# Kernel tuning notes

Hardware: AMD Instinct MI355X
Metric: run time of the kernel (lower is better)

Reference implementation:

```python
import jax, jax.numpy as jnp
import numpy as np

HEAD_DIM = 64
NUM_HEAD = 8
NUM_CLUSTERS = 16
B, N, M = 2, 2048, 2048


def setup_inputs() -> dict:
    key = jax.random.key(0)
    ks = jax.random.split(key, 10)
    d = HEAD_DIM
    inp = {
        "Q": jax.random.normal(ks[0], (B, NUM_HEAD, N, d), jnp.float32),
        "K": jax.random.normal(ks[1], (B, NUM_HEAD, M, d), jnp.float32),
        "V": jax.random.normal(ks[2], (B, NUM_HEAD, M, d), jnp.float32),
        "mask": jnp.zeros((B, M), jnp.int32),
        "noise": jax.random.uniform(ks[3], (B, NUM_HEAD, N, M), jnp.float32),
        "emb": jax.random.normal(ks[4], (NUM_HEAD * NUM_CLUSTERS, d), jnp.float32),
        "W1": jax.random.normal(ks[5], (d, d), jnp.float32) * 0.02,
        "b1": jnp.zeros((d,), jnp.float32),
        "W2": jax.random.normal(ks[6], (d, d), jnp.float32) * 0.02,
        "b2": jnp.zeros((d,), jnp.float32),
        "W3": jax.random.normal(ks[7], (d, d), jnp.float32) * 0.02,
        "b3": jnp.zeros((d,), jnp.float32),
    }
    return inp


def _proj(x, W1, b1, W2, b2, W3, b3):
    # torch nn.Linear: y = x @ W.T + b; dropout is identity in eval mode
    x = jax.nn.relu(jnp.einsum("bhnd,ed->bhne", x, W1) + b1)
    x = jax.nn.relu(jnp.einsum("bhnd,ed->bhne", x, W2) + b2)
    return jnp.einsum("bhnd,ed->bhne", x, W3) + b3


def reference(Q, K, V, mask, noise, emb, W1, b1, W2, b2, W3, b3):
    b, h, n, d = Q.shape
    m = V.shape[2]
    k = NUM_CLUSTERS

    clusters = emb.reshape(h, k, d)                                  # [h,k,d]
    dist = jnp.einsum("hkd,hjd->hkj", clusters, clusters)            # [h,k,k]
    # softmax over the flattened k*k matrix per head
    S = jax.nn.softmax(dist.reshape(h, k * k), axis=-1).reshape(h, k, k)

    Qhat = jax.nn.sigmoid(jnp.einsum("bhnd,hkd->bhnk", _proj(Q, W1, b1, W2, b2, W3, b3), clusters))
    Khat = jax.nn.sigmoid(jnp.einsum("bhmd,hkd->bhmk", _proj(K, W1, b1, W2, b2, W3, b3), clusters))

    SK = jnp.einsum("hkj,bhmj->bhkm", S, Khat)                       # [b,h,k,m]
    expA = jnp.einsum("bhnk,bhkm->bhnm", Qhat, SK)                   # Bernoulli probs in [0,1]

    # SampleGraphSparseGraph: Bernoulli sample with straight-through gradient
    sample = (noise < expA).astype(Q.dtype)
    graph = expA + jax.lax.stop_gradient(sample - expA)

    dot = jnp.einsum("bhnd,bhmd->bhnm", Q, K) / jnp.sqrt(jnp.asarray(d, Q.dtype))
    dot = jnp.where(mask[:, None, None, :] == 1, -jnp.inf, dot)
    p = jax.nn.softmax(dot, axis=-1) * graph
    # F.normalize(p=1): x / max(||x||_1, 1e-12); p is non-negative
    attn = p / jnp.maximum(jnp.sum(p, axis=-1, keepdims=True), 1e-12)

    X = jnp.einsum("bhnm,bhmd->bhnd", attn, V)
    sparsity = jnp.sum(graph, axis=(0, -1, -2)) / (b * n * m)        # [h]
    return X, sparsity, graph, attn
```

## Files before the change

kernel.cpp:

```cpp
#include <hip/hip_runtime.h>


typedef float  f32x4 __attribute__((ext_vector_type(4)));
typedef float  f32x8 __attribute__((ext_vector_type(8)));
typedef double f64x2 __attribute__((ext_vector_type(2)));
typedef __bf16 bf16x8 __attribute__((ext_vector_type(8)));

__device__ __forceinline__ unsigned short f2bf(float f) {
  __bf16 b = (__bf16)f;
  return __builtin_bit_cast(unsigned short, b);
}
__device__ __forceinline__ float bf2f(unsigned short u) {
  return (float)__builtin_bit_cast(__bf16, u);
}

__global__ __launch_bounds__(256) void kS(const float* __restrict__ emb,
                                          double* __restrict__ wsS,
                                          float* __restrict__ wsSP) {
  __shared__ double c[16][65];
  __shared__ double red[256];
  const int t = threadIdx.x, h = blockIdx.x;
  if (t == 0) wsSP[h] = 0.f;
  for (int i = t; i < 1024; i += 256) c[i >> 6][i & 63] = (double)emb[(size_t)h * 1024 + i];
  __syncthreads();
  const int k = t >> 4, j = t & 15;
  double acc = 0.0;
  for (int d = 0; d < 64; ++d) acc += c[k][d] * c[j][d];
  red[t] = acc; __syncthreads();
  for (int s = 128; s > 0; s >>= 1) { if (t < s) red[t] = fmax(red[t], red[t + s]); __syncthreads(); }
  const double mx = red[0]; __syncthreads();
  const double e = exp(acc - mx);
  red[t] = e; __syncthreads();
  for (int s = 128; s > 0; s >>= 1) { if (t < s) red[t] += red[t + s]; __syncthreads(); }
  wsS[h * 256 + t] = e / red[0];
}

__global__ __launch_bounds__(256) void kMLP(
    const float* __restrict__ Q, const float* __restrict__ K,
    const float* __restrict__ emb,
    const float* __restrict__ W1, const float* __restrict__ b1,
    const float* __restrict__ W2, const float* __restrict__ b2,
    const float* __restrict__ W3, const float* __restrict__ b3,
    const double* __restrict__ wsS,
    double* __restrict__ QHAT, double* __restrict__ SKT) {
  __shared__ double Xt[64][66];
  __shared__ float  Wl[64][68];
  __shared__ float  bsS[64];
  __shared__ float  cl[16][68];
  __shared__ double kh[64][17];
  __shared__ double Sl[256];

  const int t = threadIdx.x;
  const int blk = blockIdx.x;
  const int side = blk >> 9;
  const int idx = blk & 511;
  const int bh = idx >> 5;
  const int h = bh & 7;
  const int chunk = idx & 31;
  const size_t t0 = (size_t)bh * 2048 + (size_t)chunk * 64;

  const float* src = side ? K : Q;
  for (int i = t; i < 4096; i += 256) Xt[i >> 6][i & 63] = (double)src[t0 * 64 + i];

  const float* Ws[3] = {W1, W2, W3};
  const float* bs[3] = {b1, b2, b3};
  const int te = t & 15, tt = t >> 4;
  const int e0 = te * 4, tok0 = tt * 4;

  for (int l = 0; l < 3; ++l) {
    __syncthreads();
    for (int i = t; i < 4096; i += 256) Wl[i >> 6][i & 63] = Ws[l][i];
    if (t < 64) bsS[t] = bs[l][t];
    __syncthreads();
    double o[4][4];
#pragma unroll
    for (int i = 0; i < 4; ++i)
#pragma unroll
      for (int j = 0; j < 4; ++j) o[i][j] = 0.0;
    for (int d = 0; d < 64; d += 4) {
      double xa[4][4];
#pragma unroll
      for (int i = 0; i < 4; ++i) {
        const f64x2 lo = *(const f64x2*)&Xt[tok0 + i][d];
        const f64x2 hi = *(const f64x2*)&Xt[tok0 + i][d + 2];
        xa[i][0] = lo[0]; xa[i][1] = lo[1]; xa[i][2] = hi[0]; xa[i][3] = hi[1];
      }
      float4 wb[4];
#pragma unroll
      for (int j = 0; j < 4; ++j) wb[j] = *(const float4*)&Wl[e0 + j][d];
#pragma unroll
      for (int dd = 0; dd < 4; ++dd) {
        const double w0 = (double)((dd == 0) ? wb[0].x : (dd == 1) ? wb[0].y : (dd == 2) ? wb[0].z : wb[0].w);
        const double w1 = (double)((dd == 0) ? wb[1].x : (dd == 1) ? wb[1].y : (dd == 2) ? wb[1].z : wb[1].w);
        const double w2 = (double)((dd == 0) ? wb[2].x : (dd == 1) ? wb[2].y : (dd == 2) ? wb[2].z : wb[2].w);
        const double w3 = (double)((dd == 0) ? wb[3].x : (dd == 1) ? wb[3].y : (dd == 2) ? wb[3].z : wb[3].w);
#pragma unroll
        for (int i = 0; i < 4; ++i) {
          const double xv = xa[i][dd];
          o[i][0] += xv * w0; o[i][1] += xv * w1; o[i][2] += xv * w2; o[i][3] += xv * w3;
        }
      }
    }
#pragma unroll
    for (int i = 0; i < 4; ++i)
#pragma unroll
      for (int j = 0; j < 4; ++j) {
        double v = o[i][j] + (double)bsS[e0 + j];
        if (l < 2) v = fmax(v, 0.0);
        o[i][j] = v;
      }
    __syncthreads();
#pragma unroll
    for (int i = 0; i < 4; ++i)
#pragma unroll
      for (int j = 0; j < 4; ++j) Xt[tok0 + i][e0 + j] = o[i][j];
  }
  __syncthreads();
  for (int i = t; i < 1024; i += 256) cl[i >> 6][i & 63] = emb[(size_t)h * 1024 + i];
  if (side) { for (int i = t; i < 256; i += 256) Sl[i] = wsS[h * 256 + i]; }
  __syncthreads();

  const int tok = t >> 2, k0 = (t & 3) * 4;
  double z[4] = {0.0, 0.0, 0.0, 0.0};
  for (int d = 0; d < 64; d += 2) {
    const f64x2 xv = *(const f64x2*)&Xt[tok][d];
    const float2 c0 = *(const float2*)&cl[k0 + 0][d];
    const float2 c1 = *(const float2*)&cl[k0 + 1][d];
    const float2 c2 = *(const float2*)&cl[k0 + 2][d];
    const float2 c3 = *(const float2*)&cl[k0 + 3][d];
    z[0] += xv[0] * (double)c0.x; z[1] += xv[0] * (double)c1.x;
    z[2] += xv[0] * (double)c2.x; z[3] += xv[0] * (double)c3.x;
    z[0] += xv[1] * (double)c0.y; z[1] += xv[1] * (double)c1.y;
    z[2] += xv[1] * (double)c2.y; z[3] += xv[1] * (double)c3.y;
  }
  double hat[4];
#pragma unroll
  for (int j = 0; j < 4; ++j) hat[j] = 1.0 / (1.0 + exp(-z[j]));

  if (!side) {
#pragma unroll
    for (int j = 0; j < 4; ++j) QHAT[(t0 + tok) * 16 + k0 + j] = hat[j];
  } else {
    kh[tok][k0 + 0] = hat[0]; kh[tok][k0 + 1] = hat[1];
    kh[tok][k0 + 2] = hat[2]; kh[tok][k0 + 3] = hat[3];
    __syncthreads();
    double sk[4] = {0.0, 0.0, 0.0, 0.0};
    for (int jj = 0; jj < 16; ++jj) {
      const double kv = kh[tok][jj];
      sk[0] += Sl[(k0 + 0) * 16 + jj] * kv; sk[1] += Sl[(k0 + 1) * 16 + jj] * kv;
      sk[2] += Sl[(k0 + 2) * 16 + jj] * kv; sk[3] += Sl[(k0 + 3) * 16 + jj] * kv;
    }
#pragma unroll
    for (int j = 0; j < 4; ++j) SKT[(t0 + tok) * 16 + k0 + j] = sk[j];
  }
}

__global__ __launch_bounds__(256) void kSample(
    const float* __restrict__ noise,
    const double* __restrict__ qhat, const double* __restrict__ skt,
    float* __restrict__ wsSP,
    unsigned long long* __restrict__ GB64, float* __restrict__ GOUT) {
  const int t = threadIdx.x;
  const int lane = t & 63, wave = t >> 6;
  const int nt = blockIdx.x;
  const int mt = blockIdx.y;
  const int bh = blockIdx.z, h = bh & 7;
  const int n0 = nt * 64;
  const int mA = mt * 512 + wave * 64 + lane;
  const int mB = mA + 256;

  double skvA[16], skvB[16];
  {
    const double* spA = skt + ((size_t)bh * 2048 + mA) * 16;
    const double* spB = skt + ((size_t)bh * 2048 + mB) * 16;
#pragma unroll
    for (int q = 0; q < 8; ++q) {
      *(f64x2*)(skvA + 2 * q) = *(const f64x2*)(spA + 2 * q);
      *(f64x2*)(skvB + 2 * q) = *(const f64x2*)(spB + 2 * q);
    }
  }

  const double* qbase = qhat + ((size_t)bh * 2048 + n0) * 16;
  const float* nzbase = noise + ((size_t)bh * 2048 + n0) * 2048;
  float* gobase = GOUT + ((size_t)bh * 2048 + n0) * 2048;
  unsigned long long* gbbase = GB64 + ((size_t)bh * 2048 + n0) * 32;
  const int gA = mA >> 6, gB = mB >> 6;

  int cnt = 0;
  for (int n = 0; n < 64; ++n) {
    const double* qr = qbase + (size_t)n * 16;
    double ea0 = 0.0, ea1 = 0.0;
#pragma unroll
    for (int k = 0; k < 16; ++k) {
      const double qk = qr[k];
      ea0 += qk * skvA[k];
      ea1 += qk * skvB[k];
    }
    const float nzA = nzbase[(size_t)n * 2048 + mA];
    const float nzB = nzbase[(size_t)n * 2048 + mB];
    const int g0 = ((double)nzA < ea0) ? 1 : 0;
    const int g1 = ((double)nzB < ea1) ? 1 : 0;
    cnt += g0 + g1;
    const unsigned long long b0 = __ballot(g0);
    const unsigned long long b1 = __ballot(g1);
    if (lane == 0) {
      gbbase[(size_t)n * 32 + gA] = b0;
      gbbase[(size_t)n * 32 + gB] = b1;
    }
    gobase[(size_t)n * 2048 + mA] = g0 ? 1.0f : 0.0f;
    gobase[(size_t)n * 2048 + mB] = g1 ? 1.0f : 0.0f;
  }
  cnt += __shfl_xor(cnt, 1); cnt += __shfl_xor(cnt, 2); cnt += __shfl_xor(cnt, 4);
  cnt += __shfl_xor(cnt, 8); cnt += __shfl_xor(cnt, 16); cnt += __shfl_xor(cnt, 32);
  if (lane == 0) atomicAdd(&wsSP[h], (float)cnt);
}

__global__ __launch_bounds__(256) void kCvt(const float* __restrict__ K,
                                            const float* __restrict__ V,
                                            unsigned short* __restrict__ KB,
                                            unsigned short* __restrict__ VT) {
  __shared__ float vt[128][65];
  const int t = threadIdx.x;
  const int bh = blockIdx.x, ch = blockIdx.y;
  const size_t base = ((size_t)bh * 2048 + ch * 128) * 64;
  for (int i = t; i < 8192; i += 256) {
    KB[base + i] = f2bf(K[base + i]);
    vt[i >> 6][i & 63] = V[base + i];
  }
  __syncthreads();
  const size_t vbase = (size_t)bh * 64 * 2048 + ch * 128;
  for (int i = t; i < 8192; i += 256) {
    const int d = i >> 7, mm = i & 127;
    VT[vbase + (size_t)d * 2048 + mm] = f2bf(vt[mm][d]);
  }
}

__global__ __launch_bounds__(256, 4) void kAttn(
    const float* __restrict__ Q, const int* __restrict__ maskp,
    const unsigned short* __restrict__ KB, const unsigned short* __restrict__ VT,
    const unsigned int* __restrict__ GB32,
    float* __restrict__ XOUT, float* __restrict__ AOUT) {
  __shared__ unsigned int bitsS[16][64];
  __shared__ unsigned short stageS[4][16][32];
  __shared__ float dredS[4][16];
  __shared__ float dinvS[16];
  __shared__ float xredS[16][68];

  const int t = threadIdx.x;
  const int wave = t >> 6, lane = t & 63;
  const int bh = blockIdx.y, b = bh >> 3;
  const int n0 = blockIdx.x * 16;
  const int hi2 = lane >> 4;
  const int hi8 = hi2 << 3;
  const int g4 = hi2 << 2;
  const int lm = lane & 15;

  for (int i = t; i < 1024; i += 256)
    bitsS[i >> 6][i & 63] = GB32[((size_t)bh * 2048 + n0 + (i >> 6)) * 64 + (i & 63)];
  for (int i = t; i < 16 * 68; i += 256) ((float*)xredS)[i] = 0.f;

  const float* qrow = Q + ((size_t)bh * 2048 + n0 + lm) * 64;
  bf16x8 aq[2];
#pragma unroll
  for (int hh = 0; hh < 2; ++hh) {
    const int d0 = hi8 + hh * 32;
    const f32x4 qa = *(const f32x4*)(qrow + d0);
    const f32x4 qb = *(const f32x4*)(qrow + d0 + 4);
    bf16x8 v;
    v[0] = (__bf16)qa[0]; v[1] = (__bf16)qa[1]; v[2] = (__bf16)qa[2]; v[3] = (__bf16)qa[3];
    v[4] = (__bf16)qb[0]; v[5] = (__bf16)qb[1]; v[6] = (__bf16)qb[2]; v[7] = (__bf16)qb[3];
    aq[hh] = v;
  }

  const unsigned short* kbp = KB + (size_t)bh * 2048 * 64;
  const unsigned short* vtp = VT + (size_t)bh * 64 * 2048;
  const int* mkp = maskp + b * 2048;
  __syncthreads();

  float dsum[4] = {0.f, 0.f, 0.f, 0.f};
  for (int it = 0; it < 16; ++it) {
    const int mb = (wave << 9) + (it << 5);
    f32x4 st[2];
#pragma unroll
    for (int tt = 0; tt < 2; ++tt) {
      const unsigned short* kr = kbp + (size_t)(mb + tt * 16 + lm) * 64 + hi8;
      const bf16x8 b0 = *(const bf16x8*)(kr);
      const bf16x8 b1 = *(const bf16x8*)(kr + 32);
      f32x4 acc = (f32x4){0.f, 0.f, 0.f, 0.f};
      acc = __builtin_amdgcn_mfma_f32_16x16x32_bf16(aq[0], b0, acc, 0, 0, 0);
      acc = __builtin_amdgcn_mfma_f32_16x16x32_bf16(aq[1], b1, acc, 0, 0, 0);
      st[tt] = acc;
    }
#pragma unroll
    for (int tt = 0; tt < 2; ++tt) {
      const int mv = mkp[mb + tt * 16 + lm];
      const f32x4 sv4 = st[tt];
#pragma unroll
      for (int r = 0; r < 4; ++r) {
        const int g = (bitsS[g4 + r][mb >> 5] >> (tt * 16 + lm)) & 1;
        if (g && !mv) dsum[r] += __expf(sv4[r] * 0.125f);
      }
    }
  }
#pragma unroll
  for (int r = 0; r < 4; ++r) {
    float v = dsum[r];
    v += __shfl_xor(v, 1); v += __shfl_xor(v, 2); v += __shfl_xor(v, 4); v += __shfl_xor(v, 8);
    if (lm == 0) dredS[wave][g4 + r] = v;
  }
  __syncthreads();
  if (t < 16) {
    const float dv = dredS[0][t] + dredS[1][t] + dredS[2][t] + dredS[3][t];
    dinvS[t] = 1.0f / fmaxf(dv, 1e-12f);
  }
  __syncthreads();

  const size_t rowbase = (size_t)bh * 2048 + n0;
  f32x4 xacc[4];
#pragma unroll
  for (int td = 0; td < 4; ++td) xacc[td] = (f32x4){0.f, 0.f, 0.f, 0.f};

  for (int it = 0; it < 16; ++it) {
    const int mb = (wave << 9) + (it << 5);
    f32x4 st[2];
#pragma unroll
    for (int tt = 0; tt < 2; ++tt) {
      const unsigned short* kr = kbp + (size_t)(mb + tt * 16 + lm) * 64 + hi8;
      const bf16x8 b0 = *(const bf16x8*)(kr);
      const bf16x8 b1 = *(const bf16x8*)(kr + 32);
      f32x4 acc = (f32x4){0.f, 0.f, 0.f, 0.f};
      acc = __builtin_amdgcn_mfma_f32_16x16x32_bf16(aq[0], b0, acc, 0, 0, 0);
      acc = __builtin_amdgcn_mfma_f32_16x16x32_bf16(aq[1], b1, acc, 0, 0, 0);
      st[tt] = acc;
    }
#pragma unroll
    for (int tt = 0; tt < 2; ++tt) {
      const int mv = mkp[mb + tt * 16 + lm];
      const f32x4 sv4 = st[tt];
#pragma unroll
      for (int r = 0; r < 4; ++r) {
        const int row = g4 + r;
        const int g = (bitsS[row][mb >> 5] >> (tt * 16 + lm)) & 1;
        const float u = (g && !mv) ? __expf(sv4[r] * 0.125f) : 0.f;
        const int col = tt * 16 + lm;
        stageS[wave][row][col ^ (((row >> 2) & 3) << 3)] = f2bf(u);
      }
    }
    {
      const int rdcol = hi8 ^ (((lm >> 2) & 3) << 3);
      const bf16x8 ua = *(const bf16x8*)&stageS[wave][lm][rdcol];
#pragma unroll
      for (int td = 0; td < 4; ++td) {
        const bf16x8 vb = *(const bf16x8*)(vtp + (size_t)(td * 16 + lm) * 2048 + mb + hi8);
        xacc[td] = __builtin_amdgcn_mfma_f32_16x16x32_bf16(ua, vb, xacc[td], 0, 0, 0);
      }
    }
    {
      const int row = lane >> 2, q = lane & 3;
      const int rc = (q * 8) ^ (((row >> 2) & 3) << 3);
      const unsigned short* up = &stageS[wave][row][rc];
      const float inv = dinvS[row];
      f32x8 av;
#pragma unroll
      for (int j = 0; j < 8; ++j) av[j] = bf2f(up[j]) * inv;
      *(f32x8*)(AOUT + (rowbase + row) * 2048 + mb + q * 8) = av;
    }
  }

  for (int w = 0; w < 4; ++w) {
    if (wave == w) {
#pragma unroll
      for (int td = 0; td < 4; ++td)
#pragma unroll
        for (int r = 0; r < 4; ++r) xredS[g4 + r][td * 16 + lm] += xacc[td][r];
    }
    __syncthreads();
  }
  for (int i = t; i < 1024; i += 256) {
    const int nl = i >> 6, d = i & 63;
    XOUT[(rowbase + nl) * 64 + d] = xredS[nl][d] * dinvS[nl];
  }
}

__global__ void kFin(const float* __restrict__ wsSP, float* __restrict__ SPOUT) {
  const int t = threadIdx.x;
  if (t < 8) SPOUT[t] = wsSP[t] * (1.0f / 8388608.0f);
}

extern "C" void kernel_launch(void* const* d_in, const int* in_sizes, int n_in,
                              void* d_out, int out_size, void* d_ws, size_t ws_size,
                              hipStream_t stream) {
  const float* Q = (const float*)d_in[0];
  const float* K = (const float*)d_in[1];
  const float* V = (const float*)d_in[2];
  const int* mask = (const int*)d_in[3];
  const float* noise = (const float*)d_in[4];
  const float* emb = (const float*)d_in[5];
  const float* W1 = (const float*)d_in[6];
  const float* b1 = (const float*)d_in[7];
  const float* W2 = (const float*)d_in[8];
  const float* b2 = (const float*)d_in[9];
  const float* W3 = (const float*)d_in[10];
  const float* b3 = (const float*)d_in[11];

  char* ws = (char*)d_ws;
  double* wsS = (double*)(ws + 0);
  float* wsSP = (float*)(ws + 16384);
  double* QHAT = (double*)(ws + 32768);
  double* SKT  = (double*)(ws + 32768 + 4194304);
  unsigned short* KB = (unsigned short*)(ws + 32768);
  unsigned short* VT = (unsigned short*)(ws + 32768 + 4194304);
  unsigned long long* GB64 = (unsigned long long*)(ws + 32768 + 8388608);
  unsigned int* GB32 = (unsigned int*)(ws + 32768 + 8388608);

  float* out = (float*)d_out;
  float* XOUT = out;
  float* SPOUT = out + 2097152;
  float* GOUT = out + 2097160;
  float* AOUT = out + 69206024;

  kS<<<8, 256, 0, stream>>>(emb, wsS, wsSP);
  kMLP<<<1024, 256, 0, stream>>>(Q, K, emb, W1, b1, W2, b2, W3, b3, wsS, QHAT, SKT);
  kSample<<<dim3(32, 4, 16), 256, 0, stream>>>(noise, QHAT, SKT, wsSP, GB64, GOUT);
  kCvt<<<dim3(16, 16), 256, 0, stream>>>(K, V, KB, VT);
  kAttn<<<dim3(128, 16), 256, 0, stream>>>(Q, mask, KB, VT, GB32, XOUT, AOUT);
  kFin<<<1, 64, 0, stream>>>(wsSP, SPOUT);
}
```

Measured before the change: 506.7 us.

## Process 32 query rows per attention block to reuse K and V loads

The attention kernel now handles 32 query rows per block instead of 16, with two 16-row sub-tiles sharing each loaded K and V^T fragment across two MFMA sets. This halves the global K/V reads per query row and halves the grid size. In exchange it raises register and LDS use, which may reduce occupancy under the 4-blocks launch bound, and the smaller grid (1024 blocks) may balance less well across CUs.

After: 480.5 us. 5.2% less time.

```diff
diff --git a/kernel.cpp b/kernel.cpp
--- a/kernel.cpp
+++ b/kernel.cpp
@@ -240,36 +240,39 @@
     const unsigned short* __restrict__ KB, const unsigned short* __restrict__ VT,
     const unsigned int* __restrict__ GB32,
     float* __restrict__ XOUT, float* __restrict__ AOUT) {
-  __shared__ unsigned int bitsS[16][64];
-  __shared__ unsigned short stageS[4][16][32];
-  __shared__ float dredS[4][16];
-  __shared__ float dinvS[16];
-  __shared__ float xredS[16][68];
+  __shared__ unsigned int bitsS[32][64];
+  __shared__ unsigned short stageS[4][32][32];
+  __shared__ float dredS[4][32];
+  __shared__ float dinvS[32];
+  __shared__ float xredS[32][68];
 
   const int t = threadIdx.x;
   const int wave = t >> 6, lane = t & 63;
   const int bh = blockIdx.y, b = bh >> 3;
-  const int n0 = blockIdx.x * 16;
+  const int n0 = blockIdx.x * 32;
   const int hi2 = lane >> 4;
   const int hi8 = hi2 << 3;
   const int g4 = hi2 << 2;
   const int lm = lane & 15;
 
-  for (int i = t; i < 1024; i += 256)
+  for (int i = t; i < 2048; i += 256)
     bitsS[i >> 6][i & 63] = GB32[((size_t)bh * 2048 + n0 + (i >> 6)) * 64 + (i & 63)];
-  for (int i = t; i < 16 * 68; i += 256) ((float*)xredS)[i] = 0.f;
-
-  const float* qrow = Q + ((size_t)bh * 2048 + n0 + lm) * 64;
-  bf16x8 aq[2];
-#pragma unroll
-  for (int hh = 0; hh < 2; ++hh) {
-    const int d0 = hi8 + hh * 32;
-    const f32x4 qa = *(const f32x4*)(qrow + d0);
-    const f32x4 qb = *(const f32x4*)(qrow + d0 + 4);
-    bf16x8 v;
-    v[0] = (__bf16)qa[0]; v[1] = (__bf16)qa[1]; v[2] = (__bf16)qa[2]; v[3] = (__bf16)qa[3];
-    v[4] = (__bf16)qb[0]; v[5] = (__bf16)qb[1]; v[6] = (__bf16)qb[2]; v[7] = (__bf16)qb[3];
-    aq[hh] = v;
+  for (int i = t; i < 32 * 68; i += 256) ((float*)xredS)[i] = 0.f;
+
+  bf16x8 aq[2][2];
+#pragma unroll
+  for (int rs = 0; rs < 2; ++rs) {
+    const float* qrow = Q + ((size_t)bh * 2048 + n0 + rs * 16 + lm) * 64;
+#pragma unroll
+    for (int hh = 0; hh < 2; ++hh) {
+      const int d0 = hi8 + hh * 32;
+      const f32x4 qa = *(const f32x4*)(qrow + d0);
+      const f32x4 qb = *(const f32x4*)(qrow + d0 + 4);
+      bf16x8 v;
+      v[0] = (__bf16)qa[0]; v[1] = (__bf16)qa[1]; v[2] = (__bf16)qa[2]; v[3] = (__bf16)qa[3];
+      v[4] = (__bf16)qb[0]; v[5] = (__bf16)qb[1]; v[6] = (__bf16)qb[2]; v[7] = (__bf16)qb[3];
+      aq[rs][hh] = v;
+    }
   }
 
   const unsigned short* kbp = KB + (size_t)bh * 2048 * 64;
@@ -277,87 +280,112 @@
   const int* mkp = maskp + b * 2048;
   __syncthreads();
 
-  float dsum[4] = {0.f, 0.f, 0.f, 0.f};
+  float dsum[2][4];
+#pragma unroll
+  for (int rs = 0; rs < 2; ++rs)
+#pragma unroll
+    for (int r = 0; r < 4; ++r) dsum[rs][r] = 0.f;
+
   for (int it = 0; it < 16; ++it) {
     const int mb = (wave << 9) + (it << 5);
-    f32x4 st[2];
+    f32x4 st[2][2];
 #pragma unroll
     for (int tt = 0; tt < 2; ++tt) {
       const unsigned short* kr = kbp + (size_t)(mb + tt * 16 + lm) * 64 + hi8;
       const bf16x8 b0 = *(const bf16x8*)(kr);
       const bf16x8 b1 = *(const bf16x8*)(kr + 32);
-      f32x4 acc = (f32x4){0.f, 0.f, 0.f, 0.f};
-      acc = __builtin_amdgcn_mfma_f32_16x16x32_bf16(aq[0], b0, acc, 0, 0, 0);
-      acc = __builtin_amdgcn_mfma_f32_16x16x32_bf16(aq[1], b1, acc, 0, 0, 0);
-      st[tt] = acc;
+#pragma unroll
+      for (int rs = 0; rs < 2; ++rs) {
+        f32x4 acc = (f32x4){0.f, 0.f, 0.f, 0.f};
+        acc = __builtin_amdgcn_mfma_f32_16x16x32_bf16(aq[rs][0], b0, acc, 0, 0, 0);
+        acc = __builtin_amdgcn_mfma_f32_16x16x32_bf16(aq[rs][1], b1, acc, 0, 0, 0);
+        st[rs][tt] = acc;
+      }
     }
 #pragma unroll
     for (int tt = 0; tt < 2; ++tt) {
       const int mv = mkp[mb + tt * 16 + lm];
-      const f32x4 sv4 = st[tt];
-#pragma unroll
-      for (int r = 0; r < 4; ++r) {
-        const int g = (bitsS[g4 + r][mb >> 5] >> (tt * 16 + lm)) & 1;
-        if (g && !mv) dsum[r] += __expf(sv4[r] * 0.125f);
-      }
-    }
-  }
-#pragma unroll
-  for (int r = 0; r < 4; ++r) {
-    float v = dsum[r];
-    v += __shfl_xor(v, 1); v += __shfl_xor(v, 2); v += __shfl_xor(v, 4); v += __shfl_xor(v, 8);
-    if (lm == 0) dredS[wave][g4 + r] = v;
-  }
-  __syncthreads();
-  if (t < 16) {
+#pragma unroll
+      for (int rs = 0; rs < 2; ++rs) {
+        const f32x4 sv4 = st[rs][tt];
+#pragma unroll
+        for (int r = 0; r < 4; ++r) {
+          const int g = (bitsS[rs * 16 + g4 + r][mb >> 5] >> (tt * 16 + lm)) & 1;
+          if (g && !mv) dsum[rs][r] += __expf(sv4[r] * 0.125f);
+        }
+      }
+    }
+  }
+#pragma unroll
+  for (int rs = 0; rs < 2; ++rs)
+#pragma unroll
+    for (int r = 0; r < 4; ++r) {
+      float v = dsum[rs][r];
+      v += __shfl_xor(v, 1); v += __shfl_xor(v, 2); v += __shfl_xor(v, 4); v += __shfl_xor(v, 8);
+      if (lm == 0) dredS[wave][rs * 16 + g4 + r] = v;
+    }
+  __syncthreads();
+  if (t < 32) {
     const float dv = dredS[0][t] + dredS[1][t] + dredS[2][t] + dredS[3][t];
     dinvS[t] = 1.0f / fmaxf(dv, 1e-12f);
   }
   __syncthreads();
 
   const size_t rowbase = (size_t)bh * 2048 + n0;
-  f32x4 xacc[4];
-#pragma unroll
-  for (int td = 0; td < 4; ++td) xacc[td] = (f32x4){0.f, 0.f, 0.f, 0.f};
+  f32x4 xacc[2][4];
+#pragma unroll
+  for (int rs = 0; rs < 2; ++rs)
+#pragma unroll
+    for (int td = 0; td < 4; ++td) xacc[rs][td] = (f32x4){0.f, 0.f, 0.f, 0.f};
 
   for (int it = 0; it < 16; ++it) {
     const int mb = (wave << 9) + (it << 5);
-    f32x4 st[2];
+    f32x4 st[2][2];
 #pragma unroll
     for (int tt = 0; tt < 2; ++tt) {
       const unsigned short* kr = kbp + (size_t)(mb + tt * 16 + lm) * 64 + hi8;
       const bf16x8 b0 = *(const bf16x8*)(kr);
       const bf16x8 b1 = *(const bf16x8*)(kr + 32);
-      f32x4 acc = (f32x4){0.f, 0.f, 0.f, 0.f};
-      acc = __builtin_amdgcn_mfma_f32_16x16x32_bf16(aq[0], b0, acc, 0, 0, 0);
-      acc = __builtin_amdgcn_mfma_f32_16x16x32_bf16(aq[1], b1, acc, 0, 0, 0);
-      st[tt] = acc;
+#pragma unroll
+      for (int rs = 0; rs < 2; ++rs) {
+        f32x4 acc = (f32x4){0.f, 0.f, 0.f, 0.f};
+        acc = __builtin_amdgcn_mfma_f32_16x16x32_bf16(aq[rs][0], b0, acc, 0, 0, 0);
+        acc = __builtin_amdgcn_mfma_f32_16x16x32_bf16(aq[rs][1], b1, acc, 0, 0, 0);
+        st[rs][tt] = acc;
+      }
     }
 #pragma unroll
     for (int tt = 0; tt < 2; ++tt) {
       const int mv = mkp[mb + tt * 16 + lm];
-      const f32x4 sv4 = st[tt];
-#pragma unroll
-      for (int r = 0; r < 4; ++r) {
-        const int row = g4 + r;
-        const int g = (bitsS[row][mb >> 5] >> (tt * 16 + lm)) & 1;
-        const float u = (g && !mv) ? __expf(sv4[r] * 0.125f) : 0.f;
-        const int col = tt * 16 + lm;
-        stageS[wave][row][col ^ (((row >> 2) & 3) << 3)] = f2bf(u);
+#pragma unroll
+      for (int rs = 0; rs < 2; ++rs) {
+        const f32x4 sv4 = st[rs][tt];
+#pragma unroll
+        for (int r = 0; r < 4; ++r) {
+          const int row = rs * 16 + g4 + r;
+          const int g = (bitsS[row][mb >> 5] >> (tt * 16 + lm)) & 1;
+          const float u = (g && !mv) ? __expf(sv4[r] * 0.125f) : 0.f;
+          const int col = tt * 16 + lm;
+          stageS[wave][row][col ^ (((row >> 2) & 3) << 3)] = f2bf(u);
+        }
       }
     }
     {
       const int rdcol = hi8 ^ (((lm >> 2) & 3) << 3);
-      const bf16x8 ua = *(const bf16x8*)&stageS[wave][lm][rdcol];
+      const bf16x8 ua0 = *(const bf16x8*)&stageS[wave][lm][rdcol];
+      const bf16x8 ua1 = *(const bf16x8*)&stageS[wave][16 + lm][rdcol];
 #pragma unroll
       for (int td = 0; td < 4; ++td) {
         const bf16x8 vb = *(const bf16x8*)(vtp + (size_t)(td * 16 + lm) * 2048 + mb + hi8);
-        xacc[td] = __builtin_amdgcn_mfma_f32_16x16x32_bf16(ua, vb, xacc[td], 0, 0, 0);
-      }
-    }
-    {
-      const int row = lane >> 2, q = lane & 3;
-      const int rc = (q * 8) ^ (((row >> 2) & 3) << 3);
+        xacc[0][td] = __builtin_amdgcn_mfma_f32_16x16x32_bf16(ua0, vb, xacc[0][td], 0, 0, 0);
+        xacc[1][td] = __builtin_amdgcn_mfma_f32_16x16x32_bf16(ua1, vb, xacc[1][td], 0, 0, 0);
+      }
+    }
+#pragma unroll
+    for (int rs = 0; rs < 2; ++rs) {
+      const int row4 = lane >> 2, q = lane & 3;
+      const int row = rs * 16 + row4;
+      const int rc = (q * 8) ^ (((row4 >> 2) & 3) << 3);
       const unsigned short* up = &stageS[wave][row][rc];
       const float inv = dinvS[row];
       f32x8 av;
@@ -370,13 +398,16 @@
   for (int w = 0; w < 4; ++w) {
     if (wave == w) {
 #pragma unroll
-      for (int td = 0; td < 4; ++td)
-#pragma unroll
-        for (int r = 0; r < 4; ++r) xredS[g4 + r][td * 16 + lm] += xacc[td][r];
+      for (int rs = 0; rs < 2; ++rs)
+#pragma unroll
+        for (int td = 0; td < 4; ++td)
+#pragma unroll
+          for (int r = 0; r < 4; ++r)
+            xredS[rs * 16 + g4 + r][td * 16 + lm] += xacc[rs][td][r];
     }
     __syncthreads();
   }
-  for (int i = t; i < 1024; i += 256) {
+  for (int i = t; i < 2048; i += 256) {
     const int nl = i >> 6, d = i & 63;
     XOUT[(rowbase + nl) * 64 + d] = xredS[nl][d] * dinvS[nl];
   }
@@ -423,6 +454,6 @@
   kMLP<<<1024, 256, 0, stream>>>(Q, K, emb, W1, b1, W2, b2, W3, b3, wsS, QHAT, SKT);
   kSample<<<dim3(32, 4, 16), 256, 0, stream>>>(noise, QHAT, SKT, wsSP, GB64, GOUT);
   kCvt<<<dim3(16, 16), 256, 0, stream>>>(K, V, KB, VT);
-  kAttn<<<dim3(128, 16), 256, 0, stream>>>(Q, mask, KB, VT, GB32, XOUT, AOUT);
+  kAttn<<<dim3(64, 16), 256, 0, stream>>>(Q, mask, KB, VT, GB32, XOUT, AOUT);
   kFin<<<1, 64, 0, stream>>>(wsSP, SPOUT);
 }
```
